# Kernel optimization log

Hardware: AMD Instinct MI355X
Metric: run time of the kernel (lower is better)

## Reference

```python
import jax, jax.numpy as jnp
import numpy as np

B, N, D_MODEL, H, DK, DV = 8, 512, 512, 8, 64, 64
MAX_DIST = 512
NUM_REL = 2 * MAX_DIST - 1  # 1023


def setup_inputs() -> dict:
    key = jax.random.key(0)
    ks = jax.random.split(key, 12)
    s = 0.02
    return {
        "X": jax.random.normal(ks[0], (B, N, D_MODEL), jnp.float32),
        "Wq": jax.random.normal(ks[1], (D_MODEL, H * DK), jnp.float32) * s,
        "bq": jnp.zeros((H * DK,), jnp.float32),
        "Wk": jax.random.normal(ks[2], (D_MODEL, H * DK), jnp.float32) * s,
        "bk": jnp.zeros((H * DK,), jnp.float32),
        "Wv": jax.random.normal(ks[3], (D_MODEL, H * DV), jnp.float32) * s,
        "bv": jnp.zeros((H * DV,), jnp.float32),
        "Wo": jax.random.normal(ks[4], (H * DV, D_MODEL), jnp.float32) * s,
        "bo": jnp.zeros((D_MODEL,), jnp.float32),
        "P_k": jax.random.normal(ks[5], (NUM_REL, H), jnp.float32),
        "P_v": jax.random.normal(ks[6], (NUM_REL, H, DV), jnp.float32),
    }


def reference(X, Wq, bq, Wk, bk, Wv, bv, Wo, bo, P_k, P_v):
    b, n, d = X.shape
    scale = 1.0 / jnp.sqrt(jnp.float32(DK))
    # projections -> [b, h, n, d]
    Q = (X @ Wq + bq).reshape(b, n, H, DK).transpose(0, 2, 1, 3)
    K = (X @ Wk + bk).reshape(b, n, H, DK).transpose(0, 2, 1, 3)
    V = (X @ Wv + bv).reshape(b, n, H, DV).transpose(0, 2, 1, 3)
    # relative index: rel[i, j] = zero_offset + (j - i)
    zero_offset = NUM_REL // 2
    rel = zero_offset + (jnp.arange(n)[None, :] - jnp.arange(n)[:, None])  # [n, n]
    A_k = P_k[rel]  # [n, n, h]
    scores = (jnp.einsum("bhid,bhjd->bhij", Q, K) + A_k.transpose(2, 0, 1)[None]) * scale
    attn = jax.nn.softmax(scores, axis=-1)  # [b, h, n, n]
    # standard value mixing + relative value mixing (einsum avoids the
    # explicit [b,h,n,n,dv] broadcast the torch code materializes; same math)
    A_v = P_v[rel]  # [n, n, h, dv]
    out = jnp.einsum("bhij,bhjd->bhid", attn, V) + jnp.einsum("bhij,ijhd->bhid", attn, A_v)
    out = out.transpose(0, 2, 1, 3).reshape(b, n, H * DV)
    return out @ Wo + bo
```

## Files before the change

### kernel.cpp

```cpp
#include <hip/hip_runtime.h>
#include <math.h>

#define Bc 8
#define Nseq 512
#define DM 512
#define Hh 8
#define NUMREL 1023
#define ZOFF 511
#define STR 568

typedef short bf16x8 __attribute__((ext_vector_type(8)));
typedef float f32x4 __attribute__((ext_vector_type(4)));

__device__ __forceinline__ unsigned short f2bf(float f) {
  unsigned u = __builtin_bit_cast(unsigned, f);
  u += 0x7fff + ((u >> 16) & 1);
  return (unsigned short)(u >> 16);
}
__device__ __forceinline__ float bf2f(unsigned short h) {
  unsigned u = ((unsigned)h) << 16;
  return __builtin_bit_cast(float, u);
}

typedef __attribute__((address_space(3))) unsigned int as3_uint;
typedef __attribute__((address_space(1))) const unsigned int as1_uint;
__device__ __forceinline__ void gl_lds16(const void* g, void* l) {
  __builtin_amdgcn_global_load_lds((as1_uint*)g, (as3_uint*)l, 16, 0, 0);
}

#define WAITVM(n)                                     \
  do {                                                \
    __builtin_amdgcn_sched_barrier(0);                \
    __builtin_amdgcn_s_waitcnt(0x0F70 | (n));         \
    __builtin_amdgcn_sched_barrier(0);                \
  } while (0)
#define WAITLGKM()                                    \
  do {                                                \
    __builtin_amdgcn_sched_barrier(0);                \
    __builtin_amdgcn_s_waitcnt(0xC07F);               \
    __builtin_amdgcn_sched_barrier(0);                \
  } while (0)

__global__ __launch_bounds__(256) void prep_xF(const float* __restrict__ X,
                                               unsigned short* __restrict__ XbF) {
  const int w = threadIdx.x >> 6, lane = threadIdx.x & 63;
  const int r = blockIdx.x * 4 + w;
  const float* src = X + (size_t)r * DM + lane * 8;
  float4 a = *(const float4*)src;
  float4 b = *(const float4*)(src + 4);
  ushort4 o0, o1;
  o0.x = f2bf(a.x); o0.y = f2bf(a.y); o0.z = f2bf(a.z); o0.w = f2bf(a.w);
  o1.x = f2bf(b.x); o1.y = f2bf(b.y); o1.z = f2bf(b.z); o1.w = f2bf(b.w);
  const int mc = r >> 4, kf = lane >> 2, l = (lane & 3) * 16 + (r & 15);
  size_t flat = (((size_t)mc * 16 + kf) * 64 + l) * 8;
  *(ushort4*)(XbF + flat) = o0;
  *(ushort4*)(XbF + flat + 4) = o1;
}

__global__ __launch_bounds__(256) void prep_wF(const float* __restrict__ Wq,
                                               const float* __restrict__ Wk,
                                               const float* __restrict__ Wv,
                                               const float* __restrict__ Wo,
                                               unsigned short* __restrict__ WqF,
                                               unsigned short* __restrict__ WkF,
                                               unsigned short* __restrict__ WvF,
                                               unsigned short* __restrict__ WoFh,
                                               unsigned short* __restrict__ WoFl) {
  const int z = blockIdx.z;
  const float* src = z == 0 ? Wq : z == 1 ? Wk : z == 2 ? Wv : Wo;
  unsigned short* dst = z == 0 ? WqF : z == 1 ? WkF : z == 2 ? WvF : z == 3 ? WoFh : WoFl;
  const int k0 = blockIdx.y * 32, n0 = blockIdx.x * 32;
  __shared__ float t[32][33];
  const int tid = threadIdx.x;
#pragma unroll
  for (int u = 0; u < 4; ++u) {
    int idx = u * 256 + tid, r = idx >> 5, c = idx & 31;
    t[r][c] = src[(size_t)(k0 + r) * DM + n0 + c];
  }
  __syncthreads();
  const int ncl = tid >> 7, l = (tid >> 1) & 63, eh = tid & 1;
  const int nl = ncl * 16 + (l & 15);
  const int klb = (l >> 4) * 8 + eh * 4;
  ushort4 o;
  {
    float v0 = t[klb + 0][nl], v1 = t[klb + 1][nl], v2 = t[klb + 2][nl], v3 = t[klb + 3][nl];
    unsigned short h0 = f2bf(v0), h1 = f2bf(v1), h2 = f2bf(v2), h3 = f2bf(v3);
    if (z == 4) {
      h0 = f2bf(v0 - bf2f(h0)); h1 = f2bf(v1 - bf2f(h1));
      h2 = f2bf(v2 - bf2f(h2)); h3 = f2bf(v3 - bf2f(h3));
    }
    o.x = h0; o.y = h1; o.z = h2; o.w = h3;
  }
  size_t flat = (((size_t)((n0 >> 4) + ncl) * 16 + (k0 >> 5)) * 64 + l) * 8 + eh * 4;
  *(ushort4*)(dst + flat) = o;
}

__global__ __launch_bounds__(256) void pk_trans(const float* __restrict__ Pk,
                                                float* __restrict__ Pkt) {
  const int h = blockIdx.y;
  const int g = blockIdx.x * 256 + threadIdx.x;
  if (g < 1040)
    Pkt[(size_t)h * 1040 + g] = (g < NUMREL) ? Pk[(size_t)g * Hh + h] : 0.f;
}

__global__ __launch_bounds__(256) void pv_fragprep(const float* __restrict__ Pv,
                                                   unsigned short* __restrict__ PvF2) {
  const int g0 = blockIdx.x * 64, h = blockIdx.y;
  __shared__ float t[80][64];
  const int tid = threadIdx.x;
#pragma unroll
  for (int u = 0; u < 20; ++u) {
    int idx = u * 256 + tid, r = idx >> 6, c = idx & 63;
    int g = g0 + r;
    t[r][c] = (g < NUMREL) ? Pv[(size_t)g * 512 + h * 64 + c] : 0.f;
  }
  __syncthreads();
#pragma unroll
  for (int av = 0; av < 2; ++av)
#pragma unroll
    for (int gtl = 0; gtl < 2; ++gtl) {
      int gt = (g0 >> 5) + gtl;
#pragma unroll
      for (int dt = 0; dt < 4; ++dt) {
        size_t base = ((((size_t)av * Hh + h) * 4 + dt) * 32 + gt) * 512;
        int idx = tid * 2;
        int l = idx >> 3, e = idx & 7;
        int gr = av * 16 + gtl * 32 + (l >> 4) * 8 + e;
        int dcol = dt * 16 + (l & 15);
        ushort2 o;
        o.x = f2bf(t[gr][dcol]);
        o.y = f2bf(t[gr + 1][dcol]);
        *(ushort2*)(PvF2 + base + idx) = o;
      }
    }
}

__global__ __launch_bounds__(256, 2) void gemm_qkv(const unsigned short* __restrict__ XbF,
                                                   const unsigned short* __restrict__ WqF,
                                                   const unsigned short* __restrict__ WkF,
                                                   const unsigned short* __restrict__ WvF,
                                                   const float* __restrict__ bq,
                                                   const float* __restrict__ bk,
                                                   const float* __restrict__ bv,
                                                   unsigned short* __restrict__ Qb,
                                                   unsigned short* __restrict__ KF,
                                                   unsigned short* __restrict__ VF) {
  const int flat = blockIdx.x;
  const int xcd = flat & 7, g = flat >> 3;
  const int by = xcd * 8 + (g & 7), bx = g >> 3;
  const int bm = by * 64, bn = bx * 64;
  const int mc0 = bm >> 4, nc0 = bn >> 4;
  const int tid = threadIdx.x, w = tid >> 6, lane = tid & 63;
  const int lo = lane & 15, quad = lane >> 4;
  const int mh = (w >> 1) * 2, nh = (w & 1) * 2;

  __shared__ __align__(16) unsigned short stg[2][16 * 512];

  const unsigned short* srcArr = w == 0 ? XbF : w == 1 ? WqF : w == 2 ? WkF : WvF;
  const int rowbase = (w == 0) ? mc0 : nc0;

#define STAGE(buf, kf)                                                          \
  do {                                                                          \
    _Pragma("unroll") for (int t = 0; t < 4; ++t) {                             \
      gl_lds16(srcArr + (((size_t)(rowbase + t) * 16 + (kf)) * 512) + lane * 8, \
               &stg[buf][(w * 4 + t) * 512]);                                   \
    }                                                                           \
  } while (0)

  f32x4 acc[3][2][2] = {};
  STAGE(0, 0);
  int cur = 0;
#pragma unroll
  for (int kf = 0; kf < 16; ++kf) {
    __syncthreads();
    if (kf < 15) STAGE(cur ^ 1, kf + 1);
    bf16x8 af[2], bq_[2], bk_[2], bv_[2];
#pragma unroll
    for (int i = 0; i < 2; ++i)
      af[i] = *(const bf16x8*)(&stg[cur][(mh + i) * 512 + lane * 8]);
#pragma unroll
    for (int j = 0; j < 2; ++j) {
      bq_[j] = *(const bf16x8*)(&stg[cur][(4 + nh + j) * 512 + lane * 8]);
      bk_[j] = *(const bf16x8*)(&stg[cur][(8 + nh + j) * 512 + lane * 8]);
      bv_[j] = *(const bf16x8*)(&stg[cur][(12 + nh + j) * 512 + lane * 8]);
    }
#pragma unroll
    for (int i = 0; i < 2; ++i)
#pragma unroll
      for (int j = 0; j < 2; ++j) {
        acc[0][i][j] = __builtin_amdgcn_mfma_f32_16x16x32_bf16(af[i], bq_[j], acc[0][i][j], 0, 0, 0);
        acc[1][i][j] = __builtin_amdgcn_mfma_f32_16x16x32_bf16(af[i], bk_[j], acc[1][i][j], 0, 0, 0);
        acc[2][i][j] = __builtin_amdgcn_mfma_f32_16x16x32_bf16(af[i], bv_[j], acc[2][i][j], 0, 0, 0);
      }
    cur ^= 1;
  }
#undef STAGE

  const int mt = (w >> 1) * 32, nt = (w & 1) * 32;
#pragma unroll
  for (int z = 0; z < 3; ++z) {
    const float* bias = z == 0 ? bq : z == 1 ? bk : bv;
#pragma unroll
    for (int i = 0; i < 2; ++i)
#pragma unroll
      for (int j = 0; j < 2; ++j) {
        int col = bn + nt + j * 16 + lo;
        int h = col >> 6, d = col & 63;
        float bb = bias[col];
#pragma unroll
        for (int r = 0; r < 4; ++r) {
          int row = bm + mt + i * 16 + quad * 4 + r;
          int b = row >> 9, is = row & 511;
          int bh = b * Hh + h;
          unsigned short val = f2bf(acc[z][i][j][r] + bb);
          if (z == 0) {
            Qb[((size_t)bh * Nseq + is) * 64 + d] = val;
          } else if (z == 1) {
            int jt = is >> 4, kf2 = d >> 5, l = ((d >> 3) & 3) * 16 + (is & 15), e = d & 7;
            KF[(((size_t)bh * 32 + jt) * 2 + kf2) * 512 + l * 8 + e] = val;
          } else {
            int dt = d >> 4, ks = is >> 5, l = ((is >> 3) & 3) * 16 + (d & 15), e = is & 7;
            VF[(((size_t)bh * 4 + dt) * 16 + ks) * 512 + l * 8 + e] = val;
          }
        }
      }
  }
}

__global__ __launch_bounds__(256, 2) void attn_fused(
    const unsigned short* __restrict__ Qb,
    const unsigned short* __restrict__ KF,
    const unsigned short* __restrict__ VF,
    const float* __restrict__ Pkt,
    const unsigned short* __restrict__ PvF2,
    unsigned short* __restrict__ AwFh,
    unsigned short* __restrict__ AwFl) {
  const int flat = blockIdx.x;
  const int h = flat & 7;
  const int grp = flat >> 3;
  const int b = grp >> 4;
  const int p = grp & 15;
  const int itA = (p >> 1) * 4 + (p & 1);
  const int i0A = itA * 16;
  const int i0B = i0A + 32;
  const int bh = b * Hh + h;
  const int tid = threadIdx.x, w = tid >> 6, lane = tid & 63;
  const int lo = lane & 15, quad = lane >> 4;

  __shared__ __align__(16) unsigned short stg[2][16 * 512];
  __shared__ __align__(16) unsigned short pstA[16 * STR];
  __shared__ __align__(16) unsigned short pstB[16 * STR];
  __shared__ float pk_lds[560];
  __shared__ float redm[2][4][16];
  __shared__ float redl[2][4][16];

  const int TB = ZOFF - i0B - 15;

  int4 z4; z4.x = z4.y = z4.z = z4.w = 0;
  for (int c = tid; c < 16 * STR / 8; c += 256) {
    ((int4*)pstA)[c] = z4;
    ((int4*)pstB)[c] = z4;
  }
  for (int c = tid; c < 140; c += 256)
    *(float4*)(pk_lds + c * 4) = *(const float4*)(Pkt + (size_t)h * 1040 + TB + c * 4);

  const unsigned short* qA = Qb + ((size_t)bh * Nseq + i0A + lo) * 64;
  const unsigned short* qB = Qb + ((size_t)bh * Nseq + i0B + lo) * 64;
  bf16x8 qa0 = *(const bf16x8*)(qA + quad * 8);
  bf16x8 qa1 = *(const bf16x8*)(qA + 32 + quad * 8);
  bf16x8 qb0 = *(const bf16x8*)(qB + quad * 8);
  bf16x8 qb1 = *(const bf16x8*)(qB + 32 + quad * 8);

  const unsigned short* KFb = KF + (size_t)bh * 64 * 512;
  const unsigned short* VFb = VF + ((size_t)bh * 4 + w) * 16 * 512;
  const int aP = (TB >> 4) & 1, gtB = TB >> 5;
  const unsigned short* PFb = PvF2 + ((((size_t)aP * Hh + h) * 4 + w) * 32 + gtB) * 512;

#define KSTAGE(g, buf)                                                        \
  do {                                                                        \
    _Pragma("unroll") for (int c = 0; c < 4; ++c) {                           \
      int s_ = 2 * (g) + (c >> 1), kf_ = c & 1, jt_ = w * 8 + s_;             \
      gl_lds16(KFb + ((size_t)jt_ * 2 + kf_) * 512 + lane * 8,                \
               &stg[buf][(w * 4 + c) * 512]);                                 \
    }                                                                         \
  } while (0)
#define VSTAGE(g, buf)                                                        \
  do {                                                                        \
    _Pragma("unroll") for (int c = 0; c < 4; ++c) {                           \
      gl_lds16(VFb + ((size_t)(4 * (g) + c)) * 512 + lane * 8,                \
               &stg[buf][(w * 4 + c) * 512]);                                 \
    }                                                                         \
  } while (0)
#define PSTAGE(g, buf, n)                                                     \
  do {                                                                        \
    _Pragma("unroll") for (int c = 0; c < (n); ++c) {                         \
      gl_lds16(PFb + ((size_t)(4 * (g) + c)) * 512 + lane * 8,                \
               &stg[buf][(w * 4 + c) * 512]);                                 \
    }                                                                         \
  } while (0)

  KSTAGE(0, 0);
  KSTAGE(1, 1);
  __builtin_amdgcn_sched_barrier(0);
  __syncthreads();

  float svA[8][4], svB[8][4];
  float mA[4] = {-1e30f, -1e30f, -1e30f, -1e30f};
  float mB[4] = {-1e30f, -1e30f, -1e30f, -1e30f};
#pragma unroll
  for (int g = 0; g < 4; ++g) {
    if (g >= 2) WAITVM(4);
    bf16x8 k00 = *(const bf16x8*)(&stg[g & 1][(w * 4 + 0) * 512 + lane * 8]);
    bf16x8 k01 = *(const bf16x8*)(&stg[g & 1][(w * 4 + 1) * 512 + lane * 8]);
    bf16x8 k10 = *(const bf16x8*)(&stg[g & 1][(w * 4 + 2) * 512 + lane * 8]);
    bf16x8 k11 = *(const bf16x8*)(&stg[g & 1][(w * 4 + 3) * 512 + lane * 8]);
    WAITLGKM();
    if (g == 0) KSTAGE(2, 0);
    else if (g == 1) KSTAGE(3, 1);
    else if (g == 2) VSTAGE(0, 0);
    else VSTAGE(1, 1);
    __builtin_amdgcn_sched_barrier(0);
#pragma unroll
    for (int u = 0; u < 2; ++u) {
      int s = 2 * g + u;
      f32x4 cA = {0.f, 0.f, 0.f, 0.f};
      f32x4 cB = {0.f, 0.f, 0.f, 0.f};
      cA = __builtin_amdgcn_mfma_f32_16x16x32_bf16(qa0, u ? k10 : k00, cA, 0, 0, 0);
      cA = __builtin_amdgcn_mfma_f32_16x16x32_bf16(qa1, u ? k11 : k01, cA, 0, 0, 0);
      cB = __builtin_amdgcn_mfma_f32_16x16x32_bf16(qb0, u ? k10 : k00, cB, 0, 0, 0);
      cB = __builtin_amdgcn_mfma_f32_16x16x32_bf16(qb1, u ? k11 : k01, cB, 0, 0, 0);
      int j = w * 128 + s * 16 + lo;
#pragma unroll
      for (int r = 0; r < 4; ++r) {
        int rl = quad * 4 + r;
        int idx = j - rl + 15;
        float vA = (cA[r] + pk_lds[idx + 32]) * 0.125f;
        float vB = (cB[r] + pk_lds[idx]) * 0.125f;
        svA[s][r] = vA; svB[s][r] = vB;
        mA[r] = fmaxf(mA[r], vA);
        mB[r] = fmaxf(mB[r], vB);
      }
    }
  }

#pragma unroll
  for (int m = 1; m <= 8; m <<= 1)
#pragma unroll
    for (int r = 0; r < 4; ++r) {
      mA[r] = fmaxf(mA[r], __shfl_xor(mA[r], m));
      mB[r] = fmaxf(mB[r], __shfl_xor(mB[r], m));
    }
  if (lo == 0)
#pragma unroll
    for (int r = 0; r < 4; ++r) {
      redm[0][w][quad * 4 + r] = mA[r];
      redm[1][w][quad * 4 + r] = mB[r];
    }
  __syncthreads();
  float mfA[4], mfB[4];
#pragma unroll
  for (int r = 0; r < 4; ++r) {
    int rl = quad * 4 + r;
    mfA[r] = fmaxf(fmaxf(redm[0][0][rl], redm[0][1][rl]), fmaxf(redm[0][2][rl], redm[0][3][rl]));
    mfB[r] = fmaxf(fmaxf(redm[1][0][rl], redm[1][1][rl]), fmaxf(redm[1][2][rl], redm[1][3][rl]));
  }
  float lA[4] = {0.f, 0.f, 0.f, 0.f}, lB[4] = {0.f, 0.f, 0.f, 0.f};
#pragma unroll
  for (int s = 0; s < 8; ++s)
#pragma unroll
    for (int r = 0; r < 4; ++r) {
      float eA = __expf(svA[s][r] - mfA[r]);
      float eB = __expf(svB[s][r] - mfB[r]);
      svA[s][r] = eA; svB[s][r] = eB;
      lA[r] += eA; lB[r] += eB;
    }
#pragma unroll
  for (int m = 1; m <= 8; m <<= 1)
#pragma unroll
    for (int r = 0; r < 4; ++r) {
      lA[r] += __shfl_xor(lA[r], m);
      lB[r] += __shfl_xor(lB[r], m);
    }
  if (lo == 0)
#pragma unroll
    for (int r = 0; r < 4; ++r) {
      redl[0][w][quad * 4 + r] = lA[r];
      redl[1][w][quad * 4 + r] = lB[r];
    }
  __syncthreads();
#pragma unroll
  for (int r = 0; r < 4; ++r) {
    int rl = quad * 4 + r;
    float liA = 1.f / (redl[0][0][rl] + redl[0][1][rl] + redl[0][2][rl] + redl[0][3][rl]);
    float liB = 1.f / (redl[1][0][rl] + redl[1][1][rl] + redl[1][2][rl] + redl[1][3][rl]);
#pragma unroll
    for (int s = 0; s < 8; ++s) {
      int j = w * 128 + s * 16 + lo;
      pstA[rl * STR + 16 + j] = f2bf(svA[s][r] * liA);
      pstB[rl * STR + 16 + j] = f2bf(svB[s][r] * liB);
    }
  }
  __syncthreads();

  f32x4 oA = {0.f, 0.f, 0.f, 0.f};
  f32x4 oB = {0.f, 0.f, 0.f, 0.f};
#pragma unroll
  for (int g = 0; g < 4; ++g) {
    if (g >= 2) WAITVM(4);
    bf16x8 vb[4];
#pragma unroll
    for (int c = 0; c < 4; ++c)
      vb[c] = *(const bf16x8*)(&stg[g & 1][(w * 4 + c) * 512 + lane * 8]);
    WAITLGKM();
    if (g == 0) VSTAGE(2, 0);
    else if (g == 1) VSTAGE(3, 1);
    else if (g == 2) PSTAGE(0, 0, 4);
    else PSTAGE(1, 1, 4);
    __builtin_amdgcn_sched_barrier(0);
#pragma unroll
    for (int c = 0; c < 4; ++c) {
      int ks = 4 * g + c;
      bf16x8 pA = *(const bf16x8*)(&pstA[lo * STR + 16 + ks * 32 + quad * 8]);
      bf16x8 pB = *(const bf16x8*)(&pstB[lo * STR + 16 + ks * 32 + quad * 8]);
      oA = __builtin_amdgcn_mfma_f32_16x16x32_bf16(pA, vb[c], oA, 0, 0, 0);
      oB = __builtin_amdgcn_mfma_f32_16x16x32_bf16(pB, vb[c], oB, 0, 0, 0);
    }
  }

#pragma unroll
  for (int gp = 0; gp < 5; ++gp) {
    if (gp < 3) WAITVM(4);
    else if (gp == 3) WAITVM(2);
    else WAITVM(0);
    const int nc = (gp == 4) ? 2 : 4;
    bf16x8 pv[4];
#pragma unroll
    for (int c = 0; c < 4; ++c)
      if (c < nc)
        pv[c] = *(const bf16x8*)(&stg[gp & 1][(w * 4 + c) * 512 + lane * 8]);
    WAITLGKM();
    if (gp == 0) PSTAGE(2, 0, 4);
    else if (gp == 1) PSTAGE(3, 1, 4);
    else if (gp == 2) PSTAGE(4, 0, 2);
    __builtin_amdgcn_sched_barrier(0);
#pragma unroll
    for (int c = 0; c < 4; ++c)
      if (c < nc) {
        int cg = 4 * gp + c;
        if (cg < 17) {
          union { bf16x8 v; short s8[8]; } pa;
          int base = lo * STR + cg * 32 + quad * 8 + lo + 1;
#pragma unroll
          for (int e = 0; e < 8; ++e) pa.s8[e] = (short)pstB[base + e];
          oB = __builtin_amdgcn_mfma_f32_16x16x32_bf16(pa.v, pv[c], oB, 0, 0, 0);
        }
        if (cg >= 1) {
          union { bf16x8 v; short s8[8]; } pa;
          int base = lo * STR + (cg - 1) * 32 + quad * 8 + lo + 1;
#pragma unroll
          for (int e = 0; e < 8; ++e) pa.s8[e] = (short)pstA[base + e];
          oA = __builtin_amdgcn_mfma_f32_16x16x32_bf16(pa.v, pv[c], oA, 0, 0, 0);
        }
      }
  }

  const int kf = h * 2 + (w >> 1);
  const int lhi = ((w & 1) * 2 + (lo >> 3)) * 16;
#pragma unroll
  for (int t = 0; t < 2; ++t) {
    f32x4 o = t ? oB : oA;
    int mc = b * 32 + itA + t * 2;
#pragma unroll
    for (int r = 0; r < 4; ++r) {
      float ov = o[r];
      unsigned short hi = f2bf(ov);
      unsigned short lov = f2bf(ov - bf2f(hi));
      size_t fl = (((size_t)mc * 16 + kf) * 64 + lhi + quad * 4 + r) * 8 + (lo & 7);
      AwFh[fl] = hi;
      AwFl[fl] = lov;
    }
  }
#undef KSTAGE
#undef VSTAGE
#undef PSTAGE
}

__global__ __launch_bounds__(256, 2) void gemm_final(const unsigned short* __restrict__ AhF,
                                                     const unsigned short* __restrict__ AlF,
                                                     const unsigned short* __restrict__ BhF,
                                                     const unsigned short* __restrict__ BlF,
                                                     const float* __restrict__ bo,
                                                     float* __restrict__ out) {
  const int flat = blockIdx.x;
  const int xcd = flat & 7, g = flat >> 3;
  const int by = xcd * 8 + (g & 7), bx = g >> 3;
  const int bm = by * 64, bn = bx * 64;
  const int mc0 = bm >> 4, nc0 = bn >> 4;
  const int tid = threadIdx.x, w = tid >> 6, lane = tid & 63;
  const int lo = lane & 15, quad = lane >> 4;
  const int mh = (w >> 1) * 2, nh = (w & 1) * 2;

  __shared__ __align__(16) unsigned short stg[2][16 * 512];

  const unsigned short* srcArr = w == 0 ? AhF : w == 1 ? AlF : w == 2 ? BhF : BlF;
  const int rowbase = (w < 2) ? mc0 : nc0;

#define STAGE2(buf, kf)                                                         \
  do {                                                                          \
    _Pragma("unroll") for (int t = 0; t < 4; ++t) {                             \
      gl_lds16(srcArr + (((size_t)(rowbase + t) * 16 + (kf)) * 512) + lane * 8, \
               &stg[buf][(w * 4 + t) * 512]);                                   \
    }                                                                           \
  } while (0)

  f32x4 acc[2][2] = {};
  STAGE2(0, 0);
  int cur = 0;
#pragma unroll
  for (int kf = 0; kf < 16; ++kf) {
    __syncthreads();
    if (kf < 15) STAGE2(cur ^ 1, kf + 1);
    bf16x8 ah[2], al[2], bh[2], bl[2];
#pragma unroll
    for (int i = 0; i < 2; ++i) {
      ah[i] = *(const bf16x8*)(&stg[cur][(mh + i) * 512 + lane * 8]);
      al[i] = *(const bf16x8*)(&stg[cur][(4 + mh + i) * 512 + lane * 8]);
    }
#pragma unroll
    for (int j = 0; j < 2; ++j) {
      bh[j] = *(const bf16x8*)(&stg[cur][(8 + nh + j) * 512 + lane * 8]);
      bl[j] = *(const bf16x8*)(&stg[cur][(12 + nh + j) * 512 + lane * 8]);
    }
#pragma unroll
    for (int i = 0; i < 2; ++i)
#pragma unroll
      for (int j = 0; j < 2; ++j) {
        acc[i][j] = __builtin_amdgcn_mfma_f32_16x16x32_bf16(ah[i], bh[j], acc[i][j], 0, 0, 0);
        acc[i][j] = __builtin_amdgcn_mfma_f32_16x16x32_bf16(ah[i], bl[j], acc[i][j], 0, 0, 0);
        acc[i][j] = __builtin_amdgcn_mfma_f32_16x16x32_bf16(al[i], bh[j], acc[i][j], 0, 0, 0);
      }
    cur ^= 1;
  }
#undef STAGE2

  const int mt = (w >> 1) * 32, nt = (w & 1) * 32;
#pragma unroll
  for (int i = 0; i < 2; ++i)
#pragma unroll
    for (int j = 0; j < 2; ++j) {
      int col = bn + nt + j * 16 + lo;
      float bb = bo[col];
#pragma unroll
      for (int r = 0; r < 4; ++r) {
        int row = bm + mt + i * 16 + quad * 4 + r;
        out[(size_t)row * DM + col] = acc[i][j][r] + bb;
      }
    }
}

extern "C" void kernel_launch(void* const* d_in, const int* in_sizes, int n_in,
                              void* d_out, int out_size, void* d_ws, size_t ws_size,
                              hipStream_t stream) {
  const float* X  = (const float*)d_in[0];
  const float* Wq = (const float*)d_in[1];
  const float* bq = (const float*)d_in[2];
  const float* Wk = (const float*)d_in[3];
  const float* bk = (const float*)d_in[4];
  const float* Wv = (const float*)d_in[5];
  const float* bv = (const float*)d_in[6];
  const float* Wo = (const float*)d_in[7];
  const float* bo = (const float*)d_in[8];
  const float* Pk = (const float*)d_in[9];
  const float* Pv = (const float*)d_in[10];
  float* out = (float*)d_out;

  char* p = (char*)d_ws;
  const size_t szX    = (size_t)Bc * Nseq * DM * 2;
  const size_t szW    = (size_t)DM * DM * 2;
  const size_t szPkt  = (size_t)Hh * 1040 * 4;
  const size_t szPvF2 = (size_t)2 * Hh * 4 * 32 * 512 * 2;
  const size_t szQKV  = (size_t)Bc * Hh * Nseq * 64 * 2;
  unsigned short* XbF  = (unsigned short*)p; p += szX;
  unsigned short* WqF  = (unsigned short*)p; p += szW;
  unsigned short* WkF  = (unsigned short*)p; p += szW;
  unsigned short* WvF  = (unsigned short*)p; p += szW;
  unsigned short* WoFh = (unsigned short*)p; p += szW;
  unsigned short* WoFl = (unsigned short*)p; p += szW;
  float*          Pkt  = (float*)p;          p += (szPkt + 255) & ~(size_t)255;
  unsigned short* PvF2 = (unsigned short*)p; p += szPvF2;
  unsigned short* Qb   = (unsigned short*)p; p += szQKV;
  unsigned short* KF   = (unsigned short*)p; p += szQKV;
  unsigned short* VF   = (unsigned short*)p; p += szQKV;
  unsigned short* AwFh = (unsigned short*)p; p += szX;
  unsigned short* AwFl = (unsigned short*)p; p += szX;

  dim3 blk(256);
  prep_xF<<<dim3(1024), blk, 0, stream>>>(X, XbF);
  prep_wF<<<dim3(16, 16, 5), blk, 0, stream>>>(Wq, Wk, Wv, Wo, WqF, WkF, WvF, WoFh, WoFl);
  pk_trans<<<dim3(5, 8), blk, 0, stream>>>(Pk, Pkt);
  pv_fragprep<<<dim3(16, 8), blk, 0, stream>>>(Pv, PvF2);
  gemm_qkv<<<dim3(512), blk, 0, stream>>>(XbF, WqF, WkF, WvF, bq, bk, bv, Qb, KF, VF);
  attn_fused<<<dim3(1024), blk, 0, stream>>>(Qb, KF, VF, Pkt, PvF2, AwFh, AwFl);
  gemm_final<<<dim3(512), blk, 0, stream>>>(AwFh, AwFl, WoFh, WoFl, bo, out);
}
```

Baseline: 151.8 us.

## Merge prep kernels, deepen GEMM K-staging, and shrink attention LDS footprint

Folds the four preprocessing kernels into a single launch that dispatches on block index, removing three kernel launches. Both GEMMs now stage two K-fragments per pipeline step, halving the number of barriers at the cost of twice the LDS. The attention kernel cuts its staging buffer and pst stride and raises launch bounds to three blocks per CU for more occupancy. It also replaces the explicit waitcnt pipelining with a simpler per-step barrier loop, which may expose load latency.

New measurement: 147.2 us. 1.03x faster.

```diff
diff --git a/kernel.cpp b/kernel.cpp
--- a/kernel.cpp
+++ b/kernel.cpp
@@ -7,7 +7,7 @@
 #define Hh 8
 #define NUMREL 1023
 #define ZOFF 511
-#define STR 568
+#define STR 552
 
 typedef short bf16x8 __attribute__((ext_vector_type(8)));
 typedef float f32x4 __attribute__((ext_vector_type(4)));
@@ -28,111 +28,97 @@
   __builtin_amdgcn_global_load_lds((as1_uint*)g, (as3_uint*)l, 16, 0, 0);
 }
 
-#define WAITVM(n)                                     \
-  do {                                                \
-    __builtin_amdgcn_sched_barrier(0);                \
-    __builtin_amdgcn_s_waitcnt(0x0F70 | (n));         \
-    __builtin_amdgcn_sched_barrier(0);                \
-  } while (0)
-#define WAITLGKM()                                    \
-  do {                                                \
-    __builtin_amdgcn_sched_barrier(0);                \
-    __builtin_amdgcn_s_waitcnt(0xC07F);               \
-    __builtin_amdgcn_sched_barrier(0);                \
-  } while (0)
-
-__global__ __launch_bounds__(256) void prep_xF(const float* __restrict__ X,
-                                               unsigned short* __restrict__ XbF) {
-  const int w = threadIdx.x >> 6, lane = threadIdx.x & 63;
-  const int r = blockIdx.x * 4 + w;
-  const float* src = X + (size_t)r * DM + lane * 8;
-  float4 a = *(const float4*)src;
-  float4 b = *(const float4*)(src + 4);
-  ushort4 o0, o1;
-  o0.x = f2bf(a.x); o0.y = f2bf(a.y); o0.z = f2bf(a.z); o0.w = f2bf(a.w);
-  o1.x = f2bf(b.x); o1.y = f2bf(b.y); o1.z = f2bf(b.z); o1.w = f2bf(b.w);
-  const int mc = r >> 4, kf = lane >> 2, l = (lane & 3) * 16 + (r & 15);
-  size_t flat = (((size_t)mc * 16 + kf) * 64 + l) * 8;
-  *(ushort4*)(XbF + flat) = o0;
-  *(ushort4*)(XbF + flat + 4) = o1;
-}
-
-__global__ __launch_bounds__(256) void prep_wF(const float* __restrict__ Wq,
-                                               const float* __restrict__ Wk,
-                                               const float* __restrict__ Wv,
-                                               const float* __restrict__ Wo,
-                                               unsigned short* __restrict__ WqF,
-                                               unsigned short* __restrict__ WkF,
-                                               unsigned short* __restrict__ WvF,
-                                               unsigned short* __restrict__ WoFh,
-                                               unsigned short* __restrict__ WoFl) {
-  const int z = blockIdx.z;
-  const float* src = z == 0 ? Wq : z == 1 ? Wk : z == 2 ? Wv : Wo;
-  unsigned short* dst = z == 0 ? WqF : z == 1 ? WkF : z == 2 ? WvF : z == 3 ? WoFh : WoFl;
-  const int k0 = blockIdx.y * 32, n0 = blockIdx.x * 32;
-  __shared__ float t[32][33];
+__global__ __launch_bounds__(256) void prep_all(
+    const float* __restrict__ X, const float* __restrict__ Wq,
+    const float* __restrict__ Wk, const float* __restrict__ Wv,
+    const float* __restrict__ Wo, const float* __restrict__ Pk,
+    const float* __restrict__ Pv,
+    unsigned short* __restrict__ XbF, unsigned short* __restrict__ WqF,
+    unsigned short* __restrict__ WkF, unsigned short* __restrict__ WvF,
+    unsigned short* __restrict__ WoFh, unsigned short* __restrict__ WoFl,
+    float* __restrict__ Pkt, unsigned short* __restrict__ PvF2) {
+  __shared__ float tbuf[5120];
+  const int bid = blockIdx.x;
   const int tid = threadIdx.x;
-#pragma unroll
-  for (int u = 0; u < 4; ++u) {
-    int idx = u * 256 + tid, r = idx >> 5, c = idx & 31;
-    t[r][c] = src[(size_t)(k0 + r) * DM + n0 + c];
-  }
-  __syncthreads();
-  const int ncl = tid >> 7, l = (tid >> 1) & 63, eh = tid & 1;
-  const int nl = ncl * 16 + (l & 15);
-  const int klb = (l >> 4) * 8 + eh * 4;
-  ushort4 o;
-  {
-    float v0 = t[klb + 0][nl], v1 = t[klb + 1][nl], v2 = t[klb + 2][nl], v3 = t[klb + 3][nl];
-    unsigned short h0 = f2bf(v0), h1 = f2bf(v1), h2 = f2bf(v2), h3 = f2bf(v3);
-    if (z == 4) {
-      h0 = f2bf(v0 - bf2f(h0)); h1 = f2bf(v1 - bf2f(h1));
-      h2 = f2bf(v2 - bf2f(h2)); h3 = f2bf(v3 - bf2f(h3));
-    }
-    o.x = h0; o.y = h1; o.z = h2; o.w = h3;
-  }
-  size_t flat = (((size_t)((n0 >> 4) + ncl) * 16 + (k0 >> 5)) * 64 + l) * 8 + eh * 4;
-  *(ushort4*)(dst + flat) = o;
-}
-
-__global__ __launch_bounds__(256) void pk_trans(const float* __restrict__ Pk,
-                                                float* __restrict__ Pkt) {
-  const int h = blockIdx.y;
-  const int g = blockIdx.x * 256 + threadIdx.x;
-  if (g < 1040)
-    Pkt[(size_t)h * 1040 + g] = (g < NUMREL) ? Pk[(size_t)g * Hh + h] : 0.f;
-}
-
-__global__ __launch_bounds__(256) void pv_fragprep(const float* __restrict__ Pv,
-                                                   unsigned short* __restrict__ PvF2) {
-  const int g0 = blockIdx.x * 64, h = blockIdx.y;
-  __shared__ float t[80][64];
-  const int tid = threadIdx.x;
-#pragma unroll
-  for (int u = 0; u < 20; ++u) {
-    int idx = u * 256 + tid, r = idx >> 6, c = idx & 63;
-    int g = g0 + r;
-    t[r][c] = (g < NUMREL) ? Pv[(size_t)g * 512 + h * 64 + c] : 0.f;
-  }
-  __syncthreads();
-#pragma unroll
-  for (int av = 0; av < 2; ++av)
-#pragma unroll
-    for (int gtl = 0; gtl < 2; ++gtl) {
-      int gt = (g0 >> 5) + gtl;
-#pragma unroll
-      for (int dt = 0; dt < 4; ++dt) {
-        size_t base = ((((size_t)av * Hh + h) * 4 + dt) * 32 + gt) * 512;
-        int idx = tid * 2;
-        int l = idx >> 3, e = idx & 7;
-        int gr = av * 16 + gtl * 32 + (l >> 4) * 8 + e;
-        int dcol = dt * 16 + (l & 15);
-        ushort2 o;
-        o.x = f2bf(t[gr][dcol]);
-        o.y = f2bf(t[gr + 1][dcol]);
-        *(ushort2*)(PvF2 + base + idx) = o;
-      }
-    }
+
+  if (bid < 1024) {
+    const int w = tid >> 6, lane = tid & 63;
+    const int r = bid * 4 + w;
+    const float* src = X + (size_t)r * DM + lane * 8;
+    float4 a = *(const float4*)src;
+    float4 b = *(const float4*)(src + 4);
+    ushort4 o0, o1;
+    o0.x = f2bf(a.x); o0.y = f2bf(a.y); o0.z = f2bf(a.z); o0.w = f2bf(a.w);
+    o1.x = f2bf(b.x); o1.y = f2bf(b.y); o1.z = f2bf(b.z); o1.w = f2bf(b.w);
+    const int mc = r >> 4, kf = lane >> 2, l = (lane & 3) * 16 + (r & 15);
+    size_t flat = (((size_t)mc * 16 + kf) * 64 + l) * 8;
+    *(ushort4*)(XbF + flat) = o0;
+    *(ushort4*)(XbF + flat + 4) = o1;
+  } else if (bid < 2304) {
+    const int idx = bid - 1024;
+    const int z = idx >> 8, r256 = idx & 255;
+    const int bx = r256 & 15, by = r256 >> 4;
+    const float* src = z == 0 ? Wq : z == 1 ? Wk : z == 2 ? Wv : Wo;
+    unsigned short* dst = z == 0 ? WqF : z == 1 ? WkF : z == 2 ? WvF : z == 3 ? WoFh : WoFl;
+    const int k0 = by * 32, n0 = bx * 32;
+#pragma unroll
+    for (int u = 0; u < 4; ++u) {
+      int i2 = u * 256 + tid, r = i2 >> 5, c = i2 & 31;
+      tbuf[r * 33 + c] = src[(size_t)(k0 + r) * DM + n0 + c];
+    }
+    __syncthreads();
+    const int ncl = tid >> 7, l = (tid >> 1) & 63, eh = tid & 1;
+    const int nl = ncl * 16 + (l & 15);
+    const int klb = (l >> 4) * 8 + eh * 4;
+    ushort4 o;
+    {
+      float v0 = tbuf[(klb + 0) * 33 + nl], v1 = tbuf[(klb + 1) * 33 + nl];
+      float v2 = tbuf[(klb + 2) * 33 + nl], v3 = tbuf[(klb + 3) * 33 + nl];
+      unsigned short h0 = f2bf(v0), h1 = f2bf(v1), h2 = f2bf(v2), h3 = f2bf(v3);
+      if (z == 4) {
+        h0 = f2bf(v0 - bf2f(h0)); h1 = f2bf(v1 - bf2f(h1));
+        h2 = f2bf(v2 - bf2f(h2)); h3 = f2bf(v3 - bf2f(h3));
+      }
+      o.x = h0; o.y = h1; o.z = h2; o.w = h3;
+    }
+    size_t flat = (((size_t)((n0 >> 4) + ncl) * 16 + (k0 >> 5)) * 64 + l) * 8 + eh * 4;
+    *(ushort4*)(dst + flat) = o;
+  } else if (bid < 2344) {
+    const int idx = bid - 2304;
+    const int gx = idx % 5, h = idx / 5;
+    const int g = gx * 256 + tid;
+    if (g < 1040)
+      Pkt[(size_t)h * 1040 + g] = (g < NUMREL) ? Pk[(size_t)g * Hh + h] : 0.f;
+  } else {
+    const int idx = bid - 2344;
+    const int gx = idx & 15, h = idx >> 4;
+    const int g0 = gx * 64;
+#pragma unroll
+    for (int u = 0; u < 20; ++u) {
+      int i2 = u * 256 + tid, r = i2 >> 6, c = i2 & 63;
+      int g = g0 + r;
+      tbuf[r * 64 + c] = (g < NUMREL) ? Pv[(size_t)g * 512 + h * 64 + c] : 0.f;
+    }
+    __syncthreads();
+#pragma unroll
+    for (int av = 0; av < 2; ++av)
+#pragma unroll
+      for (int gtl = 0; gtl < 2; ++gtl) {
+        int gt = (g0 >> 5) + gtl;
+#pragma unroll
+        for (int dt = 0; dt < 4; ++dt) {
+          size_t base = ((((size_t)av * Hh + h) * 4 + dt) * 32 + gt) * 512;
+          int i2 = tid * 2;
+          int l = i2 >> 3, e = i2 & 7;
+          int gr = av * 16 + gtl * 32 + (l >> 4) * 8 + e;
+          int dcol = dt * 16 + (l & 15);
+          ushort2 o;
+          o.x = f2bf(tbuf[gr * 64 + dcol]);
+          o.y = f2bf(tbuf[(gr + 1) * 64 + dcol]);
+          *(ushort2*)(PvF2 + base + i2) = o;
+        }
+      }
+  }
 }
 
 __global__ __launch_bounds__(256, 2) void gemm_qkv(const unsigned short* __restrict__ XbF,
@@ -154,44 +140,49 @@
   const int lo = lane & 15, quad = lane >> 4;
   const int mh = (w >> 1) * 2, nh = (w & 1) * 2;
 
-  __shared__ __align__(16) unsigned short stg[2][16 * 512];
+  __shared__ __align__(16) unsigned short stg[2][32 * 512];
 
   const unsigned short* srcArr = w == 0 ? XbF : w == 1 ? WqF : w == 2 ? WkF : WvF;
   const int rowbase = (w == 0) ? mc0 : nc0;
 
-#define STAGE(buf, kf)                                                          \
-  do {                                                                          \
-    _Pragma("unroll") for (int t = 0; t < 4; ++t) {                             \
-      gl_lds16(srcArr + (((size_t)(rowbase + t) * 16 + (kf)) * 512) + lane * 8, \
-               &stg[buf][(w * 4 + t) * 512]);                                   \
-    }                                                                           \
+#define STAGE(buf, ks)                                                             \
+  do {                                                                             \
+    _Pragma("unroll") for (int t = 0; t < 8; ++t) {                                \
+      gl_lds16(srcArr +                                                            \
+                   (((size_t)(rowbase + (t >> 1)) * 16 + 2 * (ks) + (t & 1)) * 512) + \
+                   lane * 8,                                                       \
+               &stg[buf][(w * 8 + t) * 512]);                                      \
+    }                                                                              \
   } while (0)
 
   f32x4 acc[3][2][2] = {};
   STAGE(0, 0);
   int cur = 0;
 #pragma unroll
-  for (int kf = 0; kf < 16; ++kf) {
-    __syncthreads();
-    if (kf < 15) STAGE(cur ^ 1, kf + 1);
-    bf16x8 af[2], bq_[2], bk_[2], bv_[2];
-#pragma unroll
-    for (int i = 0; i < 2; ++i)
-      af[i] = *(const bf16x8*)(&stg[cur][(mh + i) * 512 + lane * 8]);
-#pragma unroll
-    for (int j = 0; j < 2; ++j) {
-      bq_[j] = *(const bf16x8*)(&stg[cur][(4 + nh + j) * 512 + lane * 8]);
-      bk_[j] = *(const bf16x8*)(&stg[cur][(8 + nh + j) * 512 + lane * 8]);
-      bv_[j] = *(const bf16x8*)(&stg[cur][(12 + nh + j) * 512 + lane * 8]);
-    }
-#pragma unroll
-    for (int i = 0; i < 2; ++i)
+  for (int ks = 0; ks < 8; ++ks) {
+    __syncthreads();
+    if (ks < 7) STAGE(cur ^ 1, ks + 1);
+#pragma unroll
+    for (int kf = 0; kf < 2; ++kf) {
+      bf16x8 af[2], bq_[2], bk_[2], bv_[2];
+#pragma unroll
+      for (int i = 0; i < 2; ++i)
+        af[i] = *(const bf16x8*)(&stg[cur][((mh + i) * 2 + kf) * 512 + lane * 8]);
 #pragma unroll
       for (int j = 0; j < 2; ++j) {
-        acc[0][i][j] = __builtin_amdgcn_mfma_f32_16x16x32_bf16(af[i], bq_[j], acc[0][i][j], 0, 0, 0);
-        acc[1][i][j] = __builtin_amdgcn_mfma_f32_16x16x32_bf16(af[i], bk_[j], acc[1][i][j], 0, 0, 0);
-        acc[2][i][j] = __builtin_amdgcn_mfma_f32_16x16x32_bf16(af[i], bv_[j], acc[2][i][j], 0, 0, 0);
-      }
+        bq_[j] = *(const bf16x8*)(&stg[cur][(8 + (nh + j) * 2 + kf) * 512 + lane * 8]);
+        bk_[j] = *(const bf16x8*)(&stg[cur][(16 + (nh + j) * 2 + kf) * 512 + lane * 8]);
+        bv_[j] = *(const bf16x8*)(&stg[cur][(24 + (nh + j) * 2 + kf) * 512 + lane * 8]);
+      }
+#pragma unroll
+      for (int i = 0; i < 2; ++i)
+#pragma unroll
+        for (int j = 0; j < 2; ++j) {
+          acc[0][i][j] = __builtin_amdgcn_mfma_f32_16x16x32_bf16(af[i], bq_[j], acc[0][i][j], 0, 0, 0);
+          acc[1][i][j] = __builtin_amdgcn_mfma_f32_16x16x32_bf16(af[i], bk_[j], acc[1][i][j], 0, 0, 0);
+          acc[2][i][j] = __builtin_amdgcn_mfma_f32_16x16x32_bf16(af[i], bv_[j], acc[2][i][j], 0, 0, 0);
+        }
+    }
     cur ^= 1;
   }
 #undef STAGE
@@ -227,7 +218,7 @@
   }
 }
 
-__global__ __launch_bounds__(256, 2) void attn_fused(
+__global__ __launch_bounds__(256, 3) void attn_fused(
     const unsigned short* __restrict__ Qb,
     const unsigned short* __restrict__ KF,
     const unsigned short* __restrict__ VF,
@@ -242,19 +233,16 @@
   const int p = grp & 15;
   const int itA = (p >> 1) * 4 + (p & 1);
   const int i0A = itA * 16;
-  const int i0B = i0A + 32;
   const int bh = b * Hh + h;
   const int tid = threadIdx.x, w = tid >> 6, lane = tid & 63;
   const int lo = lane & 15, quad = lane >> 4;
 
-  __shared__ __align__(16) unsigned short stg[2][16 * 512];
+  __shared__ __align__(16) unsigned short stg[2][4096];
   __shared__ __align__(16) unsigned short pstA[16 * STR];
   __shared__ __align__(16) unsigned short pstB[16 * STR];
   __shared__ float pk_lds[560];
-  __shared__ float redm[2][4][16];
-  __shared__ float redl[2][4][16];
-
-  const int TB = ZOFF - i0B - 15;
+
+  const int TB = 464 - i0A;
 
   int4 z4; z4.x = z4.y = z4.z = z4.w = 0;
   for (int c = tid; c < 16 * STR / 8; c += 256) {
@@ -265,7 +253,7 @@
     *(float4*)(pk_lds + c * 4) = *(const float4*)(Pkt + (size_t)h * 1040 + TB + c * 4);
 
   const unsigned short* qA = Qb + ((size_t)bh * Nseq + i0A + lo) * 64;
-  const unsigned short* qB = Qb + ((size_t)bh * Nseq + i0B + lo) * 64;
+  const unsigned short* qB = Qb + ((size_t)bh * Nseq + i0A + 32 + lo) * 64;
   bf16x8 qa0 = *(const bf16x8*)(qA + quad * 8);
   bf16x8 qa1 = *(const bf16x8*)(qA + 32 + quad * 8);
   bf16x8 qb0 = *(const bf16x8*)(qB + quad * 8);
@@ -276,73 +264,58 @@
   const int aP = (TB >> 4) & 1, gtB = TB >> 5;
   const unsigned short* PFb = PvF2 + ((((size_t)aP * Hh + h) * 4 + w) * 32 + gtB) * 512;
 
-#define KSTAGE(g, buf)                                                        \
-  do {                                                                        \
-    _Pragma("unroll") for (int c = 0; c < 4; ++c) {                           \
-      int s_ = 2 * (g) + (c >> 1), kf_ = c & 1, jt_ = w * 8 + s_;             \
-      gl_lds16(KFb + ((size_t)jt_ * 2 + kf_) * 512 + lane * 8,                \
-               &stg[buf][(w * 4 + c) * 512]);                                 \
-    }                                                                         \
+#define KSTAGE(g, buf)                                                     \
+  do {                                                                     \
+    _Pragma("unroll") for (int c = 0; c < 2; ++c)                          \
+        gl_lds16(KFb + ((size_t)(w * 8 + (g)) * 2 + c) * 512 + lane * 8,   \
+                 &stg[buf][(w * 2 + c) * 512]);                            \
   } while (0)
-#define VSTAGE(g, buf)                                                        \
-  do {                                                                        \
-    _Pragma("unroll") for (int c = 0; c < 4; ++c) {                           \
-      gl_lds16(VFb + ((size_t)(4 * (g) + c)) * 512 + lane * 8,                \
-               &stg[buf][(w * 4 + c) * 512]);                                 \
-    }                                                                         \
+#define VSTAGE(g, buf)                                                     \
+  do {                                                                     \
+    _Pragma("unroll") for (int c = 0; c < 2; ++c)                          \
+        gl_lds16(VFb + ((size_t)(2 * (g) + c)) * 512 + lane * 8,           \
+                 &stg[buf][(w * 2 + c) * 512]);                            \
   } while (0)
-#define PSTAGE(g, buf, n)                                                     \
-  do {                                                                        \
-    _Pragma("unroll") for (int c = 0; c < (n); ++c) {                         \
-      gl_lds16(PFb + ((size_t)(4 * (g) + c)) * 512 + lane * 8,                \
-               &stg[buf][(w * 4 + c) * 512]);                                 \
-    }                                                                         \
+#define PSTAGE(g, buf)                                                     \
+  do {                                                                     \
+    _Pragma("unroll") for (int c = 0; c < 2; ++c)                          \
+        gl_lds16(PFb + ((size_t)(2 * (g) + c)) * 512 + lane * 8,           \
+                 &stg[buf][(w * 2 + c) * 512]);                            \
   } while (0)
 
   KSTAGE(0, 0);
-  KSTAGE(1, 1);
-  __builtin_amdgcn_sched_barrier(0);
   __syncthreads();
 
   float svA[8][4], svB[8][4];
   float mA[4] = {-1e30f, -1e30f, -1e30f, -1e30f};
   float mB[4] = {-1e30f, -1e30f, -1e30f, -1e30f};
 #pragma unroll
-  for (int g = 0; g < 4; ++g) {
-    if (g >= 2) WAITVM(4);
-    bf16x8 k00 = *(const bf16x8*)(&stg[g & 1][(w * 4 + 0) * 512 + lane * 8]);
-    bf16x8 k01 = *(const bf16x8*)(&stg[g & 1][(w * 4 + 1) * 512 + lane * 8]);
-    bf16x8 k10 = *(const bf16x8*)(&stg[g & 1][(w * 4 + 2) * 512 + lane * 8]);
-    bf16x8 k11 = *(const bf16x8*)(&stg[g & 1][(w * 4 + 3) * 512 + lane * 8]);
-    WAITLGKM();
-    if (g == 0) KSTAGE(2, 0);
-    else if (g == 1) KSTAGE(3, 1);
-    else if (g == 2) VSTAGE(0, 0);
-    else VSTAGE(1, 1);
-    __builtin_amdgcn_sched_barrier(0);
-#pragma unroll
-    for (int u = 0; u < 2; ++u) {
-      int s = 2 * g + u;
-      f32x4 cA = {0.f, 0.f, 0.f, 0.f};
-      f32x4 cB = {0.f, 0.f, 0.f, 0.f};
-      cA = __builtin_amdgcn_mfma_f32_16x16x32_bf16(qa0, u ? k10 : k00, cA, 0, 0, 0);
-      cA = __builtin_amdgcn_mfma_f32_16x16x32_bf16(qa1, u ? k11 : k01, cA, 0, 0, 0);
-      cB = __builtin_amdgcn_mfma_f32_16x16x32_bf16(qb0, u ? k10 : k00, cB, 0, 0, 0);
-      cB = __builtin_amdgcn_mfma_f32_16x16x32_bf16(qb1, u ? k11 : k01, cB, 0, 0, 0);
-      int j = w * 128 + s * 16 + lo;
-#pragma unroll
-      for (int r = 0; r < 4; ++r) {
-        int rl = quad * 4 + r;
-        int idx = j - rl + 15;
-        float vA = (cA[r] + pk_lds[idx + 32]) * 0.125f;
-        float vB = (cB[r] + pk_lds[idx]) * 0.125f;
-        svA[s][r] = vA; svB[s][r] = vB;
-        mA[r] = fmaxf(mA[r], vA);
-        mB[r] = fmaxf(mB[r], vB);
-      }
-    }
-  }
-
+  for (int g = 0; g < 8; ++g) {
+    bf16x8 k0 = *(const bf16x8*)(&stg[g & 1][(w * 2 + 0) * 512 + lane * 8]);
+    bf16x8 k1 = *(const bf16x8*)(&stg[g & 1][(w * 2 + 1) * 512 + lane * 8]);
+    if (g < 7) KSTAGE(g + 1, (g + 1) & 1);
+    f32x4 cA = {0.f, 0.f, 0.f, 0.f};
+    f32x4 cB = {0.f, 0.f, 0.f, 0.f};
+    cA = __builtin_amdgcn_mfma_f32_16x16x32_bf16(qa0, k0, cA, 0, 0, 0);
+    cA = __builtin_amdgcn_mfma_f32_16x16x32_bf16(qa1, k1, cA, 0, 0, 0);
+    cB = __builtin_amdgcn_mfma_f32_16x16x32_bf16(qb0, k0, cB, 0, 0, 0);
+    cB = __builtin_amdgcn_mfma_f32_16x16x32_bf16(qb1, k1, cB, 0, 0, 0);
+    int j = w * 128 + g * 16 + lo;
+#pragma unroll
+    for (int r = 0; r < 4; ++r) {
+      int rl = quad * 4 + r;
+      int idx = j - rl + 15;
+      float vA = (cA[r] + pk_lds[idx + 32]) * 0.125f;
+      float vB = (cB[r] + pk_lds[idx]) * 0.125f;
+      svA[g][r] = vA; svB[g][r] = vB;
+      mA[r] = fmaxf(mA[r], vA);
+      mB[r] = fmaxf(mB[r], vB);
+    }
+    __syncthreads();
+  }
+
+  float* redm = (float*)&stg[1][0];
+  float* redl = (float*)&stg[1][256];
 #pragma unroll
   for (int m = 1; m <= 8; m <<= 1)
 #pragma unroll
@@ -353,16 +326,16 @@
   if (lo == 0)
 #pragma unroll
     for (int r = 0; r < 4; ++r) {
-      redm[0][w][quad * 4 + r] = mA[r];
-      redm[1][w][quad * 4 + r] = mB[r];
+      redm[(0 * 4 + w) * 16 + quad * 4 + r] = mA[r];
+      redm[(1 * 4 + w) * 16 + quad * 4 + r] = mB[r];
     }
   __syncthreads();
   float mfA[4], mfB[4];
 #pragma unroll
   for (int r = 0; r < 4; ++r) {
     int rl = quad * 4 + r;
-    mfA[r] = fmaxf(fmaxf(redm[0][0][rl], redm[0][1][rl]), fmaxf(redm[0][2][rl], redm[0][3][rl]));
-    mfB[r] = fmaxf(fmaxf(redm[1][0][rl], redm[1][1][rl]), fmaxf(redm[1][2][rl], redm[1][3][rl]));
+    mfA[r] = fmaxf(fmaxf(redm[rl], redm[16 + rl]), fmaxf(redm[32 + rl], redm[48 + rl]));
+    mfB[r] = fmaxf(fmaxf(redm[64 + rl], redm[80 + rl]), fmaxf(redm[96 + rl], redm[112 + rl]));
   }
   float lA[4] = {0.f, 0.f, 0.f, 0.f}, lB[4] = {0.f, 0.f, 0.f, 0.f};
 #pragma unroll
@@ -384,15 +357,15 @@
   if (lo == 0)
 #pragma unroll
     for (int r = 0; r < 4; ++r) {
-      redl[0][w][quad * 4 + r] = lA[r];
-      redl[1][w][quad * 4 + r] = lB[r];
+      redl[(0 * 4 + w) * 16 + quad * 4 + r] = lA[r];
+      redl[(1 * 4 + w) * 16 + quad * 4 + r] = lB[r];
     }
   __syncthreads();
 #pragma unroll
   for (int r = 0; r < 4; ++r) {
     int rl = quad * 4 + r;
-    float liA = 1.f / (redl[0][0][rl] + redl[0][1][rl] + redl[0][2][rl] + redl[0][3][rl]);
-    float liB = 1.f / (redl[1][0][rl] + redl[1][1][rl] + redl[1][2][rl] + redl[1][3][rl]);
+    float liA = 1.f / (redl[rl] + redl[16 + rl] + redl[32 + rl] + redl[48 + rl]);
+    float liB = 1.f / (redl[64 + rl] + redl[80 + rl] + redl[96 + rl] + redl[112 + rl]);
 #pragma unroll
     for (int s = 0; s < 8; ++s) {
       int j = w * 128 + s * 16 + lo;
@@ -400,68 +373,65 @@
       pstB[rl * STR + 16 + j] = f2bf(svB[s][r] * liB);
     }
   }
+  VSTAGE(0, 0);
   __syncthreads();
 
   f32x4 oA = {0.f, 0.f, 0.f, 0.f};
   f32x4 oB = {0.f, 0.f, 0.f, 0.f};
 #pragma unroll
-  for (int g = 0; g < 4; ++g) {
-    if (g >= 2) WAITVM(4);
-    bf16x8 vb[4];
-#pragma unroll
-    for (int c = 0; c < 4; ++c)
-      vb[c] = *(const bf16x8*)(&stg[g & 1][(w * 4 + c) * 512 + lane * 8]);
-    WAITLGKM();
-    if (g == 0) VSTAGE(2, 0);
-    else if (g == 1) VSTAGE(3, 1);
-    else if (g == 2) PSTAGE(0, 0, 4);
-    else PSTAGE(1, 1, 4);
-    __builtin_amdgcn_sched_barrier(0);
-#pragma unroll
-    for (int c = 0; c < 4; ++c) {
-      int ks = 4 * g + c;
+  for (int g = 0; g < 8; ++g) {
+    bf16x8 v0 = *(const bf16x8*)(&stg[g & 1][(w * 2 + 0) * 512 + lane * 8]);
+    bf16x8 v1 = *(const bf16x8*)(&stg[g & 1][(w * 2 + 1) * 512 + lane * 8]);
+    if (g < 7) VSTAGE(g + 1, (g + 1) & 1);
+    else PSTAGE(0, 0);
+#pragma unroll
+    for (int c = 0; c < 2; ++c) {
+      int ks = 2 * g + c;
+      bf16x8 vv = c ? v1 : v0;
       bf16x8 pA = *(const bf16x8*)(&pstA[lo * STR + 16 + ks * 32 + quad * 8]);
       bf16x8 pB = *(const bf16x8*)(&pstB[lo * STR + 16 + ks * 32 + quad * 8]);
-      oA = __builtin_amdgcn_mfma_f32_16x16x32_bf16(pA, vb[c], oA, 0, 0, 0);
-      oB = __builtin_amdgcn_mfma_f32_16x16x32_bf16(pB, vb[c], oB, 0, 0, 0);
-    }
-  }
-
-#pragma unroll
-  for (int gp = 0; gp < 5; ++gp) {
-    if (gp < 3) WAITVM(4);
-    else if (gp == 3) WAITVM(2);
-    else WAITVM(0);
-    const int nc = (gp == 4) ? 2 : 4;
-    bf16x8 pv[4];
-#pragma unroll
-    for (int c = 0; c < 4; ++c)
-      if (c < nc)
-        pv[c] = *(const bf16x8*)(&stg[gp & 1][(w * 4 + c) * 512 + lane * 8]);
-    WAITLGKM();
-    if (gp == 0) PSTAGE(2, 0, 4);
-    else if (gp == 1) PSTAGE(3, 1, 4);
-    else if (gp == 2) PSTAGE(4, 0, 2);
-    __builtin_amdgcn_sched_barrier(0);
-#pragma unroll
-    for (int c = 0; c < 4; ++c)
-      if (c < nc) {
-        int cg = 4 * gp + c;
-        if (cg < 17) {
-          union { bf16x8 v; short s8[8]; } pa;
+      oA = __builtin_amdgcn_mfma_f32_16x16x32_bf16(pA, vv, oA, 0, 0, 0);
+      oB = __builtin_amdgcn_mfma_f32_16x16x32_bf16(pB, vv, oB, 0, 0, 0);
+    }
+    __syncthreads();
+  }
+
+#pragma unroll
+  for (int g = 0; g < 9; ++g) {
+    bf16x8 p0 = *(const bf16x8*)(&stg[g & 1][(w * 2 + 0) * 512 + lane * 8]);
+    bf16x8 p1 = *(const bf16x8*)(&stg[g & 1][(w * 2 + 1) * 512 + lane * 8]);
+    if (g < 8) PSTAGE(g + 1, (g + 1) & 1);
+#pragma unroll
+    for (int c = 0; c < 2; ++c) {
+      int cg = 2 * g + c;
+      bf16x8 pvf = c ? p1 : p0;
+      if (cg < 17) {
+        union { bf16x8 v; unsigned short s8[8]; } pa;
+        if (cg == 16 && quad >= 2) {
+#pragma unroll
+          for (int e = 0; e < 8; ++e) pa.s8[e] = 0;
+        } else {
           int base = lo * STR + cg * 32 + quad * 8 + lo + 1;
 #pragma unroll
-          for (int e = 0; e < 8; ++e) pa.s8[e] = (short)pstB[base + e];
-          oB = __builtin_amdgcn_mfma_f32_16x16x32_bf16(pa.v, pv[c], oB, 0, 0, 0);
+          for (int e = 0; e < 8; ++e) pa.s8[e] = pstB[base + e];
         }
-        if (cg >= 1) {
-          union { bf16x8 v; short s8[8]; } pa;
-          int base = lo * STR + (cg - 1) * 32 + quad * 8 + lo + 1;
-#pragma unroll
-          for (int e = 0; e < 8; ++e) pa.s8[e] = (short)pstA[base + e];
-          oA = __builtin_amdgcn_mfma_f32_16x16x32_bf16(pa.v, pv[c], oA, 0, 0, 0);
+        oB = __builtin_amdgcn_mfma_f32_16x16x32_bf16(pa.v, pvf, oB, 0, 0, 0);
+      }
+      if (cg >= 1) {
+        int ksA = cg - 1;
+        union { bf16x8 v; unsigned short s8[8]; } pa;
+        if (ksA == 16 && quad >= 2) {
+#pragma unroll
+          for (int e = 0; e < 8; ++e) pa.s8[e] = 0;
+        } else {
+          int base = lo * STR + ksA * 32 + quad * 8 + lo + 1;
+#pragma unroll
+          for (int e = 0; e < 8; ++e) pa.s8[e] = pstA[base + e];
         }
-      }
+        oA = __builtin_amdgcn_mfma_f32_16x16x32_bf16(pa.v, pvf, oA, 0, 0, 0);
+      }
+    }
+    __syncthreads();
   }
 
   const int kf = h * 2 + (w >> 1);
@@ -500,45 +470,50 @@
   const int lo = lane & 15, quad = lane >> 4;
   const int mh = (w >> 1) * 2, nh = (w & 1) * 2;
 
-  __shared__ __align__(16) unsigned short stg[2][16 * 512];
+  __shared__ __align__(16) unsigned short stg[2][32 * 512];
 
   const unsigned short* srcArr = w == 0 ? AhF : w == 1 ? AlF : w == 2 ? BhF : BlF;
   const int rowbase = (w < 2) ? mc0 : nc0;
 
-#define STAGE2(buf, kf)                                                         \
-  do {                                                                          \
-    _Pragma("unroll") for (int t = 0; t < 4; ++t) {                             \
-      gl_lds16(srcArr + (((size_t)(rowbase + t) * 16 + (kf)) * 512) + lane * 8, \
-               &stg[buf][(w * 4 + t) * 512]);                                   \
-    }                                                                           \
+#define STAGE2(buf, ks)                                                            \
+  do {                                                                             \
+    _Pragma("unroll") for (int t = 0; t < 8; ++t) {                                \
+      gl_lds16(srcArr +                                                            \
+                   (((size_t)(rowbase + (t >> 1)) * 16 + 2 * (ks) + (t & 1)) * 512) + \
+                   lane * 8,                                                       \
+               &stg[buf][(w * 8 + t) * 512]);                                      \
+    }                                                                              \
   } while (0)
 
   f32x4 acc[2][2] = {};
   STAGE2(0, 0);
   int cur = 0;
 #pragma unroll
-  for (int kf = 0; kf < 16; ++kf) {
-    __syncthreads();
-    if (kf < 15) STAGE2(cur ^ 1, kf + 1);
-    bf16x8 ah[2], al[2], bh[2], bl[2];
-#pragma unroll
-    for (int i = 0; i < 2; ++i) {
-      ah[i] = *(const bf16x8*)(&stg[cur][(mh + i) * 512 + lane * 8]);
-      al[i] = *(const bf16x8*)(&stg[cur][(4 + mh + i) * 512 + lane * 8]);
-    }
-#pragma unroll
-    for (int j = 0; j < 2; ++j) {
-      bh[j] = *(const bf16x8*)(&stg[cur][(8 + nh + j) * 512 + lane * 8]);
-      bl[j] = *(const bf16x8*)(&stg[cur][(12 + nh + j) * 512 + lane * 8]);
-    }
-#pragma unroll
-    for (int i = 0; i < 2; ++i)
+  for (int ks = 0; ks < 8; ++ks) {
+    __syncthreads();
+    if (ks < 7) STAGE2(cur ^ 1, ks + 1);
+#pragma unroll
+    for (int kf = 0; kf < 2; ++kf) {
+      bf16x8 ah[2], al[2], bh[2], bl[2];
+#pragma unroll
+      for (int i = 0; i < 2; ++i) {
+        ah[i] = *(const bf16x8*)(&stg[cur][((mh + i) * 2 + kf) * 512 + lane * 8]);
+        al[i] = *(const bf16x8*)(&stg[cur][(8 + (mh + i) * 2 + kf) * 512 + lane * 8]);
+      }
 #pragma unroll
       for (int j = 0; j < 2; ++j) {
-        acc[i][j] = __builtin_amdgcn_mfma_f32_16x16x32_bf16(ah[i], bh[j], acc[i][j], 0, 0, 0);
-        acc[i][j] = __builtin_amdgcn_mfma_f32_16x16x32_bf16(ah[i], bl[j], acc[i][j], 0, 0, 0);
-        acc[i][j] = __builtin_amdgcn_mfma_f32_16x16x32_bf16(al[i], bh[j], acc[i][j], 0, 0, 0);
-      }
+        bh[j] = *(const bf16x8*)(&stg[cur][(16 + (nh + j) * 2 + kf) * 512 + lane * 8]);
+        bl[j] = *(const bf16x8*)(&stg[cur][(24 + (nh + j) * 2 + kf) * 512 + lane * 8]);
+      }
+#pragma unroll
+      for (int i = 0; i < 2; ++i)
+#pragma unroll
+        for (int j = 0; j < 2; ++j) {
+          acc[i][j] = __builtin_amdgcn_mfma_f32_16x16x32_bf16(ah[i], bh[j], acc[i][j], 0, 0, 0);
+          acc[i][j] = __builtin_amdgcn_mfma_f32_16x16x32_bf16(ah[i], bl[j], acc[i][j], 0, 0, 0);
+          acc[i][j] = __builtin_amdgcn_mfma_f32_16x16x32_bf16(al[i], bh[j], acc[i][j], 0, 0, 0);
+        }
+    }
     cur ^= 1;
   }
 #undef STAGE2
@@ -595,10 +570,8 @@
   unsigned short* AwFl = (unsigned short*)p; p += szX;
 
   dim3 blk(256);
-  prep_xF<<<dim3(1024), blk, 0, stream>>>(X, XbF);
-  prep_wF<<<dim3(16, 16, 5), blk, 0, stream>>>(Wq, Wk, Wv, Wo, WqF, WkF, WvF, WoFh, WoFl);
-  pk_trans<<<dim3(5, 8), blk, 0, stream>>>(Pk, Pkt);
-  pv_fragprep<<<dim3(16, 8), blk, 0, stream>>>(Pv, PvF2);
+  prep_all<<<dim3(2472), blk, 0, stream>>>(X, Wq, Wk, Wv, Wo, Pk, Pv,
+                                           XbF, WqF, WkF, WvF, WoFh, WoFl, Pkt, PvF2);
   gemm_qkv<<<dim3(512), blk, 0, stream>>>(XbF, WqF, WkF, WvF, bq, bk, bv, Qb, KF, VF);
   attn_fused<<<dim3(1024), blk, 0, stream>>>(Qb, KF, VF, Pkt, PvF2, AwFh, AwFl);
   gemm_final<<<dim3(512), blk, 0, stream>>>(AwFh, AwFl, WoFh, WoFl, bo, out);
```
